# Optimization experiments

Hardware: AMD Instinct MI355X
Metric: run time of the kernel (lower is better)

Reference implementation:

```python
import jax, jax.numpy as jnp
import numpy as np

ALPHA = 2.6
OPTIMAL_RANK = 1.0
SIGMA = 1.8


def setup_inputs() -> dict:
    key = jax.random.key(0)
    k1, k2 = jax.random.split(key)
    B, D, NP = 2048, 768, 8
    q_reps = jax.random.normal(k1, (B, D), dtype=jnp.float32)
    p_reps = jax.random.normal(k2, (B * NP, D), dtype=jnp.float32)
    return {"q_reps": q_reps, "p_reps": p_reps, "n_passages": NP}


def reference(q_reps, p_reps, n_passages):
    B = q_reps.shape[0]
    # [B, P] contrastive score matrix
    scores = jnp.matmul(q_reps, p_reps.T)
    target = jnp.arange(B, dtype=jnp.int32) * n_passages

    # rank position of the positive passage per query (descending argsort)
    rankings = jnp.argsort(-scores, axis=1)            # [B, P]
    positive_rankings = jnp.argmax(
        rankings == target[:, None], axis=1
    ).astype(jnp.float32)                              # [B]

    # per-sample cross-entropy (reduction='none')
    logp = jax.nn.log_softmax(scores, axis=1)
    raw_loss = -jnp.take_along_axis(logp, target[:, None], axis=1)[:, 0]

    # Gaussian rank weighting: w = 1 + alpha * exp(-(r - r_opt)^2 / (2 sigma^2))
    extra_weight = jnp.exp(-((positive_rankings - OPTIMAL_RANK) ** 2) / (2.0 * SIGMA ** 2))
    weights = 1.0 + ALPHA * extra_weight

    loss = jnp.mean(raw_loss * weights)
    return loss
```

## Files before the change

kernel.cpp:

```cpp
#include <hip/hip_runtime.h>
#include <math.h>


#define BQ 2048
#define DD 768
#define NPASS 8
#define PP 16384
#define BM 256
#define BN 256
#define BK 64
#define KITERS 12
#define NBLK 64
#define MBLK 8
#define NCHUNKS 256

#define ALPHA_C 2.6f
#define INV_2SIG2 (1.0f/6.48f)

typedef __attribute__((ext_vector_type(4))) float floatx4;
typedef __attribute__((ext_vector_type(2))) long longx2;

#define NQ8   196608
#define NTOT8 1769472
#define NCB   6912
__global__ __launch_bounds__(256) void prep_kernel(const float* __restrict__ qf,
                                                   const float* __restrict__ pf,
                                                   uint2* __restrict__ qb,
                                                   uint2* __restrict__ pb,
                                                   float* __restrict__ st,
                                                   float* __restrict__ out) {
  const int b = blockIdx.x;
  if (b == 0 && threadIdx.x == 0) *out = 0.f;
  if (b < NCB) {
    const int i = b * 256 + threadIdx.x;
    const float4* src; uint2* dst;
    if (i < NQ8) { src = (const float4*)qf + 2 * (size_t)i; dst = qb + i; }
    else { const size_t j = (size_t)i - NQ8; src = (const float4*)pf + 2 * j; dst = pb + j; }
    const float4 a = src[0], c = src[1];
    unsigned lo = __builtin_amdgcn_cvt_pk_fp8_f32(a.x, a.y, 0, 0);
    lo = __builtin_amdgcn_cvt_pk_fp8_f32(a.z, a.w, lo, 1);
    unsigned hi = __builtin_amdgcn_cvt_pk_fp8_f32(c.x, c.y, 0, 0);
    hi = __builtin_amdgcn_cvt_pk_fp8_f32(c.z, c.w, hi, 1);
    uint2 w; w.x = lo; w.y = hi;
    *dst = w;
  } else {
    const int wv = threadIdx.x >> 6, lane = threadIdx.x & 63;
    const int qi = (b - NCB) * 4 + wv;
    const float4* q4 = (const float4*)(qf + (size_t)qi * DD);
    const float4* p4 = (const float4*)(pf + (size_t)qi * NPASS * DD);
    float acc = 0.f;
#pragma unroll
    for (int u = 0; u < 3; ++u) {
      float4 a = q4[lane + 64 * u];
      float4 c = p4[lane + 64 * u];
      acc = fmaf(a.x, c.x, acc);
      acc = fmaf(a.y, c.y, acc);
      acc = fmaf(a.z, c.z, acc);
      acc = fmaf(a.w, c.w, acc);
    }
#pragma unroll
    for (int off = 32; off >= 1; off >>= 1) acc += __shfl_xor(acc, off);
    if (lane == 0) st[qi] = acc;
  }
}

__global__ __launch_bounds__(1024) void gemm_kernel(const unsigned char* __restrict__ qb,
                                                    const unsigned char* __restrict__ pb,
                                                    const float* __restrict__ st,
                                                    float* __restrict__ pm,
                                                    float* __restrict__ pl,
                                                    float* __restrict__ pc) {
  __shared__ unsigned char As[3][16 * 1024];
  __shared__ unsigned char Bs[3][16 * 1024];
  __shared__ float st_lds[BM];

  const int t = threadIdx.x;
  const int lane = t & 63;
  const int wv = t >> 6;
  const int wm = wv >> 2, wn = wv & 3;
  const int bid = blockIdx.x;
  const int xcd = bid & 7;
  const int nb = xcd * 8 + ((bid >> 3) & 7);
  const int mb = bid >> 6;
  const int qbase = mb * BM;
  const int n0 = nb * BN;
  const int lm = lane & 15;
  const int lq = lane >> 4;
  const int lds_lane = lane * 16;

  if (t < BM) st_lds[t] = st[qbase + t];

  floatx4 acc[4][4];
#pragma unroll
  for (int i = 0; i < 4; ++i)
#pragma unroll
    for (int j = 0; j < 4; ++j) acc[i][j] = (floatx4){0.f, 0.f, 0.f, 0.f};

  const size_t arow = (size_t)(qbase + wv * 16 + lm) * DD;
  const size_t brow = (size_t)(n0 + wv * 16 + lm) * DD;
  const int intra16 = lq * 256 + lm * 16;

#define STAGE(KT, BUF)                                                          \
  {                                                                             \
    const size_t koff = (size_t)(KT) * BK + lq * 16;                            \
    __builtin_amdgcn_global_load_lds(                                           \
        (const __attribute__((address_space(1))) void*)(qb + arow + koff),      \
        (__attribute__((address_space(3))) void*)(&As[BUF][wv * 1024] + lds_lane), \
        16, 0, 0);                                                              \
    __builtin_amdgcn_global_load_lds(                                           \
        (const __attribute__((address_space(1))) void*)(pb + brow + koff),      \
        (__attribute__((address_space(3))) void*)(&Bs[BUF][wv * 1024] + lds_lane), \
        16, 0, 0);                                                              \
  }

#define COMPUTE(CB)                                                             \
  {                                                                             \
    longx2 a2[4], b2[4];                                                        \
    _Pragma("unroll")                                                           \
    for (int i = 0; i < 4; ++i)                                                 \
      a2[i] = *(const longx2*)(&As[CB][(wm * 4 + i) * 1024] + intra16);         \
    _Pragma("unroll")                                                           \
    for (int j = 0; j < 4; ++j)                                                 \
      b2[j] = *(const longx2*)(&Bs[CB][(wn * 4 + j) * 1024] + intra16);         \
    __builtin_amdgcn_s_setprio(1);                                              \
    _Pragma("unroll")                                                           \
    for (int i = 0; i < 4; ++i)                                                 \
      _Pragma("unroll")                                                         \
      for (int j = 0; j < 4; ++j)                                               \
        acc[i][j] = __builtin_amdgcn_mfma_f32_16x16x32_fp8_fp8(a2[i].x, b2[j].x, acc[i][j], 0, 0, 0); \
    _Pragma("unroll")                                                           \
    for (int i = 0; i < 4; ++i)                                                 \
      _Pragma("unroll")                                                         \
      for (int j = 0; j < 4; ++j)                                               \
        acc[i][j] = __builtin_amdgcn_mfma_f32_16x16x32_fp8_fp8(a2[i].y, b2[j].y, acc[i][j], 0, 0, 0); \
    __builtin_amdgcn_s_setprio(0);                                              \
  }

  STAGE(0, 0)
  STAGE(1, 1)
  int cur = 0;
  int stg = 2;
  for (int kt = 0; kt < KITERS - 1; ++kt) {
    asm volatile("s_waitcnt vmcnt(2)" ::: "memory");
    __builtin_amdgcn_s_barrier();
    __builtin_amdgcn_sched_barrier(0);
    if (kt < KITERS - 2) STAGE(kt + 2, stg)
    COMPUTE(cur)
    cur = (cur == 2) ? 0 : cur + 1;
    stg = (stg == 2) ? 0 : stg + 1;
  }
  asm volatile("s_waitcnt vmcnt(0)" ::: "memory");
  __builtin_amdgcn_s_barrier();
  __builtin_amdgcn_sched_barrier(0);
  COMPUTE(cur)

  const int chunk = nb * 4 + wn;
  float* const pmc = pm + (size_t)chunk * BQ;
  float* const plc = pl + (size_t)chunk * BQ;
  float* const pcc = pc + (size_t)chunk * BQ;
#pragma unroll
  for (int i = 0; i < 4; ++i) {
#pragma unroll
    for (int r = 0; r < 4; ++r) {
      const int rl = wm * 64 + i * 16 + lq * 4 + r;
      float mx = fmaxf(fmaxf(acc[i][0][r], acc[i][1][r]),
                       fmaxf(acc[i][2][r], acc[i][3][r]));
#pragma unroll
      for (int off = 1; off <= 8; off <<= 1) mx = fmaxf(mx, __shfl_xor(mx, off));
      const float stv = st_lds[rl];
      const int qg = qbase + rl;
      const int tcol = qg * NPASS;
      float sum = 0.f, c = 0.f;
#pragma unroll
      for (int j = 0; j < 4; ++j) {
        const float s = acc[i][j][r];
        sum += __expf(s - mx);
        const int cg = n0 + wn * 64 + j * 16 + lm;
        if (s > stv && cg != tcol) c += 1.f;
      }
#pragma unroll
      for (int off = 1; off <= 8; off <<= 1) {
        sum += __shfl_xor(sum, off);
        c += __shfl_xor(c, off);
      }
      if (lm == 0) {
        pmc[qg] = mx; plc[qg] = sum; pcc[qg] = c;
      }
    }
  }
}

__global__ __launch_bounds__(256) void finalize_kernel(const float* __restrict__ st,
                                                       const float* __restrict__ pm,
                                                       const float* __restrict__ pl,
                                                       const float* __restrict__ pc,
                                                       float* __restrict__ out) {
  const int wv = threadIdx.x >> 6, lane = threadIdx.x & 63;
  const int q = blockIdx.x * 64 + lane;
  const int c0 = wv * 64;
  float m = -1e30f, l = 0.f, c = 0.f;
#pragma unroll 4
  for (int ch = 0; ch < 64; ++ch) {
    const size_t idx = (size_t)(c0 + ch) * BQ + q;
    const float mv = pm[idx], lv = pl[idx], cv = pc[idx];
    const float nm = fmaxf(m, mv);
    l = l * __expf(m - nm) + lv * __expf(mv - nm);
    m = nm; c += cv;
  }
  __shared__ float sm[4][64], sl[4][64], sc[4][64];
  sm[wv][lane] = m; sl[wv][lane] = l; sc[wv][lane] = c;
  __syncthreads();
  if (wv == 0) {
    float M = sm[0][lane], L = sl[0][lane], C = sc[0][lane];
#pragma unroll
    for (int w = 1; w < 4; ++w) {
      const float mv = sm[w][lane];
      const float nm = fmaxf(M, mv);
      L = L * __expf(M - nm) + sl[w][lane] * __expf(mv - nm);
      M = nm; C += sc[w][lane];
    }
    const float raw = logf(L) + M - st[q];
    const float dr = C - 1.0f;
    const float w = 1.0f + ALPHA_C * __expf(-(dr * dr) * INV_2SIG2);
    float loss = raw * w * (1.0f / (float)BQ);
#pragma unroll
    for (int off = 32; off >= 1; off >>= 1) loss += __shfl_xor(loss, off);
    if (lane == 0) atomicAdd(out, loss);
  }
}

extern "C" void kernel_launch(void* const* d_in, const int* in_sizes, int n_in,
                              void* d_out, int out_size, void* d_ws, size_t ws_size,
                              hipStream_t stream) {
  const float* q = (const float*)d_in[0];
  const float* p = (const float*)d_in[1];
  char* ws = (char*)d_ws;
  unsigned char* qb = (unsigned char*)ws;
  unsigned char* pb = (unsigned char*)(ws + 1572864);
  float* st = (float*)(ws + 14155776);
  float* pm = (float*)(ws + 14163968);
  float* pl = (float*)(ws + 16261120);
  float* pc = (float*)(ws + 18358272);
  float* out = (float*)d_out;

  prep_kernel<<<NCB + BQ / 4, 256, 0, stream>>>(q, p, (uint2*)qb, (uint2*)pb, st, out);
  gemm_kernel<<<NBLK * MBLK, 1024, 0, stream>>>(qb, pb, st, pm, pl, pc);
  finalize_kernel<<<BQ / 64, 256, 0, stream>>>(st, pm, pl, pc, out);
}
```

Before: 153.2 us.

## Use 8 waves with 128x64 warp tiles and phase-interleaved staging in fp8 GEMM

Halves the block to 512 threads (8 waves) so each wave computes a 128x64 output tile with 8x4 accumulators. This doubles register-level reuse of the B fragments and lets two blocks share a CU. The K loop is split into four phases, each issuing one quarter of the next stage's global-to-LDS loads between MFMA groups to spread memory traffic. The cost is more barriers per K step and higher register pressure under the (512,2) launch bounds. The epilogue row mapping is updated to match.

New measurement: 165.0 us. 1.08x slower.

```diff
diff --git a/kernel.cpp b/kernel.cpp
--- a/kernel.cpp
+++ b/kernel.cpp
@@ -64,12 +64,12 @@
   }
 }
 
-__global__ __launch_bounds__(1024) void gemm_kernel(const unsigned char* __restrict__ qb,
-                                                    const unsigned char* __restrict__ pb,
-                                                    const float* __restrict__ st,
-                                                    float* __restrict__ pm,
-                                                    float* __restrict__ pl,
-                                                    float* __restrict__ pc) {
+__global__ __launch_bounds__(512, 2) void gemm_kernel(const unsigned char* __restrict__ qb,
+                                                      const unsigned char* __restrict__ pb,
+                                                      const float* __restrict__ st,
+                                                      float* __restrict__ pm,
+                                                      float* __restrict__ pl,
+                                                      float* __restrict__ pc) {
   __shared__ unsigned char As[3][16 * 1024];
   __shared__ unsigned char Bs[3][16 * 1024];
   __shared__ float st_lds[BM];
@@ -90,79 +90,105 @@
 
   if (t < BM) st_lds[t] = st[qbase + t];
 
-  floatx4 acc[4][4];
-#pragma unroll
-  for (int i = 0; i < 4; ++i)
+  floatx4 acc[8][4];
+#pragma unroll
+  for (int i = 0; i < 8; ++i)
 #pragma unroll
     for (int j = 0; j < 4; ++j) acc[i][j] = (floatx4){0.f, 0.f, 0.f, 0.f};
 
-  const size_t arow = (size_t)(qbase + wv * 16 + lm) * DD;
-  const size_t brow = (size_t)(n0 + wv * 16 + lm) * DD;
+  const size_t arowA = (size_t)(qbase + wv * 16 + lm) * DD;
+  const size_t arowB = arowA + (size_t)128 * DD;
+  const size_t browA = (size_t)(n0 + wv * 16 + lm) * DD;
+  const size_t browB = browA + (size_t)128 * DD;
   const int intra16 = lq * 256 + lm * 16;
 
-#define STAGE(KT, BUF)                                                          \
+#define STAGE_A0(KT, BUF)                                                       \
+  __builtin_amdgcn_global_load_lds(                                             \
+      (const __attribute__((address_space(1))) void*)(qb + arowA + (size_t)(KT) * BK + lq * 16), \
+      (__attribute__((address_space(3))) void*)(&As[BUF][wv * 1024] + lds_lane), 16, 0, 0);
+#define STAGE_A1(KT, BUF)                                                       \
+  __builtin_amdgcn_global_load_lds(                                             \
+      (const __attribute__((address_space(1))) void*)(qb + arowB + (size_t)(KT) * BK + lq * 16), \
+      (__attribute__((address_space(3))) void*)(&As[BUF][(wv + 8) * 1024] + lds_lane), 16, 0, 0);
+#define STAGE_B0(KT, BUF)                                                       \
+  __builtin_amdgcn_global_load_lds(                                             \
+      (const __attribute__((address_space(1))) void*)(pb + browA + (size_t)(KT) * BK + lq * 16), \
+      (__attribute__((address_space(3))) void*)(&Bs[BUF][wv * 1024] + lds_lane), 16, 0, 0);
+#define STAGE_B1(KT, BUF)                                                       \
+  __builtin_amdgcn_global_load_lds(                                             \
+      (const __attribute__((address_space(1))) void*)(pb + browB + (size_t)(KT) * BK + lq * 16), \
+      (__attribute__((address_space(3))) void*)(&Bs[BUF][(wv + 8) * 1024] + lds_lane), 16, 0, 0);
+
+#define MFMA16(Q)                                                               \
   {                                                                             \
-    const size_t koff = (size_t)(KT) * BK + lq * 16;                            \
-    __builtin_amdgcn_global_load_lds(                                           \
-        (const __attribute__((address_space(1))) void*)(qb + arow + koff),      \
-        (__attribute__((address_space(3))) void*)(&As[BUF][wv * 1024] + lds_lane), \
-        16, 0, 0);                                                              \
-    __builtin_amdgcn_global_load_lds(                                           \
-        (const __attribute__((address_space(1))) void*)(pb + brow + koff),      \
-        (__attribute__((address_space(3))) void*)(&Bs[BUF][wv * 1024] + lds_lane), \
-        16, 0, 0);                                                              \
-  }
-
-#define COMPUTE(CB)                                                             \
+    acc[2*Q+0][0] = __builtin_amdgcn_mfma_f32_16x16x32_fp8_fp8(a2[0].x, b2[0].x, acc[2*Q+0][0], 0, 0, 0); \
+    acc[2*Q+0][1] = __builtin_amdgcn_mfma_f32_16x16x32_fp8_fp8(a2[0].x, b2[1].x, acc[2*Q+0][1], 0, 0, 0); \
+    acc[2*Q+0][2] = __builtin_amdgcn_mfma_f32_16x16x32_fp8_fp8(a2[0].x, b2[2].x, acc[2*Q+0][2], 0, 0, 0); \
+    acc[2*Q+0][3] = __builtin_amdgcn_mfma_f32_16x16x32_fp8_fp8(a2[0].x, b2[3].x, acc[2*Q+0][3], 0, 0, 0); \
+    acc[2*Q+1][0] = __builtin_amdgcn_mfma_f32_16x16x32_fp8_fp8(a2[1].x, b2[0].x, acc[2*Q+1][0], 0, 0, 0); \
+    acc[2*Q+1][1] = __builtin_amdgcn_mfma_f32_16x16x32_fp8_fp8(a2[1].x, b2[1].x, acc[2*Q+1][1], 0, 0, 0); \
+    acc[2*Q+1][2] = __builtin_amdgcn_mfma_f32_16x16x32_fp8_fp8(a2[1].x, b2[2].x, acc[2*Q+1][2], 0, 0, 0); \
+    acc[2*Q+1][3] = __builtin_amdgcn_mfma_f32_16x16x32_fp8_fp8(a2[1].x, b2[3].x, acc[2*Q+1][3], 0, 0, 0); \
+    acc[2*Q+0][0] = __builtin_amdgcn_mfma_f32_16x16x32_fp8_fp8(a2[0].y, b2[0].y, acc[2*Q+0][0], 0, 0, 0); \
+    acc[2*Q+0][1] = __builtin_amdgcn_mfma_f32_16x16x32_fp8_fp8(a2[0].y, b2[1].y, acc[2*Q+0][1], 0, 0, 0); \
+    acc[2*Q+0][2] = __builtin_amdgcn_mfma_f32_16x16x32_fp8_fp8(a2[0].y, b2[2].y, acc[2*Q+0][2], 0, 0, 0); \
+    acc[2*Q+0][3] = __builtin_amdgcn_mfma_f32_16x16x32_fp8_fp8(a2[0].y, b2[3].y, acc[2*Q+0][3], 0, 0, 0); \
+    acc[2*Q+1][0] = __builtin_amdgcn_mfma_f32_16x16x32_fp8_fp8(a2[1].y, b2[0].y, acc[2*Q+1][0], 0, 0, 0); \
+    acc[2*Q+1][1] = __builtin_amdgcn_mfma_f32_16x16x32_fp8_fp8(a2[1].y, b2[1].y, acc[2*Q+1][1], 0, 0, 0); \
+    acc[2*Q+1][2] = __builtin_amdgcn_mfma_f32_16x16x32_fp8_fp8(a2[1].y, b2[2].y, acc[2*Q+1][2], 0, 0, 0); \
+    acc[2*Q+1][3] = __builtin_amdgcn_mfma_f32_16x16x32_fp8_fp8(a2[1].y, b2[3].y, acc[2*Q+1][3], 0, 0, 0); \
+  }
+
+#define PHASE(Q, STAGE_STMT)                                                    \
   {                                                                             \
-    longx2 a2[4], b2[4];                                                        \
-    _Pragma("unroll")                                                           \
-    for (int i = 0; i < 4; ++i)                                                 \
-      a2[i] = *(const longx2*)(&As[CB][(wm * 4 + i) * 1024] + intra16);         \
-    _Pragma("unroll")                                                           \
-    for (int j = 0; j < 4; ++j)                                                 \
-      b2[j] = *(const longx2*)(&Bs[CB][(wn * 4 + j) * 1024] + intra16);         \
+    if (Q == 0) {                                                               \
+      b2[0] = *(const longx2*)(&Bs[cur][(wn * 4 + 0) * 1024] + intra16);        \
+      b2[1] = *(const longx2*)(&Bs[cur][(wn * 4 + 1) * 1024] + intra16);        \
+      b2[2] = *(const longx2*)(&Bs[cur][(wn * 4 + 2) * 1024] + intra16);        \
+      b2[3] = *(const longx2*)(&Bs[cur][(wn * 4 + 3) * 1024] + intra16);        \
+    }                                                                           \
+    a2[0] = *(const longx2*)(&As[cur][(wm * 8 + 2 * Q + 0) * 1024] + intra16);  \
+    a2[1] = *(const longx2*)(&As[cur][(wm * 8 + 2 * Q + 1) * 1024] + intra16);  \
+    if (kt < KITERS - 2) { STAGE_STMT }                                         \
+    __builtin_amdgcn_s_barrier();                                               \
+    asm volatile("s_waitcnt lgkmcnt(0)" ::: "memory");                          \
+    __builtin_amdgcn_sched_barrier(0);                                          \
     __builtin_amdgcn_s_setprio(1);                                              \
-    _Pragma("unroll")                                                           \
-    for (int i = 0; i < 4; ++i)                                                 \
-      _Pragma("unroll")                                                         \
-      for (int j = 0; j < 4; ++j)                                               \
-        acc[i][j] = __builtin_amdgcn_mfma_f32_16x16x32_fp8_fp8(a2[i].x, b2[j].x, acc[i][j], 0, 0, 0); \
-    _Pragma("unroll")                                                           \
-    for (int i = 0; i < 4; ++i)                                                 \
-      _Pragma("unroll")                                                         \
-      for (int j = 0; j < 4; ++j)                                               \
-        acc[i][j] = __builtin_amdgcn_mfma_f32_16x16x32_fp8_fp8(a2[i].y, b2[j].y, acc[i][j], 0, 0, 0); \
+    MFMA16(Q)                                                                   \
     __builtin_amdgcn_s_setprio(0);                                              \
-  }
-
-  STAGE(0, 0)
-  STAGE(1, 1)
+    if (Q == 3) {                                                               \
+      if (kt < KITERS - 2) { asm volatile("s_waitcnt vmcnt(4)" ::: "memory"); } \
+      else                 { asm volatile("s_waitcnt vmcnt(0)" ::: "memory"); } \
+    }                                                                           \
+    __builtin_amdgcn_s_barrier();                                               \
+  }
+
+  STAGE_A0(0, 0) STAGE_A1(0, 0) STAGE_B0(0, 0) STAGE_B1(0, 0)
+  STAGE_A0(1, 1) STAGE_A1(1, 1) STAGE_B0(1, 1) STAGE_B1(1, 1)
+  asm volatile("s_waitcnt vmcnt(4)" ::: "memory");
+  __builtin_amdgcn_s_barrier();
+
   int cur = 0;
   int stg = 2;
-  for (int kt = 0; kt < KITERS - 1; ++kt) {
-    asm volatile("s_waitcnt vmcnt(2)" ::: "memory");
-    __builtin_amdgcn_s_barrier();
-    __builtin_amdgcn_sched_barrier(0);
-    if (kt < KITERS - 2) STAGE(kt + 2, stg)
-    COMPUTE(cur)
+  for (int kt = 0; kt < KITERS; ++kt) {
+    longx2 a2[2], b2[4];
+    PHASE(0, STAGE_A0(kt + 2, stg))
+    PHASE(1, STAGE_A1(kt + 2, stg))
+    PHASE(2, STAGE_B0(kt + 2, stg))
+    PHASE(3, STAGE_B1(kt + 2, stg))
     cur = (cur == 2) ? 0 : cur + 1;
     stg = (stg == 2) ? 0 : stg + 1;
   }
-  asm volatile("s_waitcnt vmcnt(0)" ::: "memory");
-  __builtin_amdgcn_s_barrier();
-  __builtin_amdgcn_sched_barrier(0);
-  COMPUTE(cur)
 
   const int chunk = nb * 4 + wn;
   float* const pmc = pm + (size_t)chunk * BQ;
   float* const plc = pl + (size_t)chunk * BQ;
   float* const pcc = pc + (size_t)chunk * BQ;
 #pragma unroll
-  for (int i = 0; i < 4; ++i) {
+  for (int i = 0; i < 8; ++i) {
 #pragma unroll
     for (int r = 0; r < 4; ++r) {
-      const int rl = wm * 64 + i * 16 + lq * 4 + r;
+      const int rl = wm * 128 + i * 16 + lq * 4 + r;
       float mx = fmaxf(fmaxf(acc[i][0][r], acc[i][1][r]),
                        fmaxf(acc[i][2][r], acc[i][3][r]));
 #pragma unroll
@@ -244,6 +270,6 @@
   float* out = (float*)d_out;
 
   prep_kernel<<<NCB + BQ / 4, 256, 0, stream>>>(q, p, (uint2*)qb, (uint2*)pb, st, out);
-  gemm_kernel<<<NBLK * MBLK, 1024, 0, stream>>>(qb, pb, st, pm, pl, pc);
+  gemm_kernel<<<NBLK * MBLK, 512, 0, stream>>>(qb, pb, st, pm, pl, pc);
   finalize_kernel<<<BQ / 64, 256, 0, stream>>>(st, pm, pl, pc, out);
 }
```
